# Kernel optimization log

Measured on AMD Instinct MI355X. Metric: run time of the kernel, lower is better.

## Reference

```python
import jax, jax.numpy as jnp
import numpy as np

BETA = 0.25
NUM_EMBEDDINGS = 512
DIM_EMBEDDING = 64


def setup_inputs() -> dict:
    key = jax.random.key(0)
    k1, k2 = jax.random.split(key)
    z_e = jax.random.normal(k1, (32, 64, 64, 64), dtype=jnp.float32)
    # torch init: uniform_(-1/num_embeddings, 1/num_embeddings)
    lim = 1.0 / NUM_EMBEDDINGS
    embeddings = jax.random.uniform(
        k2, (NUM_EMBEDDINGS, DIM_EMBEDDING), dtype=jnp.float32,
        minval=-lim, maxval=lim)
    return {"z_e": z_e, "embeddings": embeddings}


def reference(z_e, embeddings):
    # Flatten exactly as torch's z_e.view(-1, dim_embedding) on (N,C,H,W)
    z_flat = z_e.reshape(-1, DIM_EMBEDDING)          # [M, D]
    # Squared euclidean distances: ||z||^2 + ||e||^2 - 2 z e^T
    distances = (
        jnp.sum(z_flat ** 2, axis=1, keepdims=True)
        + jnp.sum(embeddings ** 2, axis=1)
        - 2.0 * jnp.matmul(z_flat, embeddings.T)
    )                                                # [M, K]
    encoding_indices = jnp.argmin(distances, axis=1)[:, None]  # [M, 1]
    quantized = embeddings[encoding_indices[:, 0]].reshape(z_e.shape)
    # Straight-through estimator
    quantized_st = z_e + jax.lax.stop_gradient(quantized - z_e)
    recon_loss = jnp.mean((jax.lax.stop_gradient(quantized_st) - z_e) ** 2)
    commitment_loss = BETA * jnp.mean(
        (quantized_st - jax.lax.stop_gradient(z_e)) ** 2)
    loss = recon_loss + commitment_loss
    return (loss, quantized_st, encoding_indices)
```

## Files before the change

### kernel.cpp

```cpp
#include <hip/hip_runtime.h>
#include <hip/hip_bf16.h>

constexpr int NELEM = 8388608;
constexpr int ROWS  = 64;
constexpr int NBLK  = 131072 / ROWS;
constexpr int ZS    = 68;
constexpr float EPS = 1e-3f;
constexpr int QCAP  = 1024;

typedef short bf16x8 __attribute__((ext_vector_type(8)));
typedef float v4f    __attribute__((ext_vector_type(4)));

__device__ bf16x8 g_efrag[32][2][64];
__device__ float  g_en2[512];

__device__ inline bf16x8 cvt_hi8(const float* __restrict__ s, float scale) {
    bf16x8 h;
#pragma unroll
    for (int j = 0; j < 8; ++j) {
        __hip_bfloat16 b = __float2bfloat16(scale * s[j]);
        h[j] = (short)__bfloat16_as_ushort(b);
    }
    return h;
}

__global__ void __launch_bounds__(256) vq_prep(const float* __restrict__ emb,
                                               float* __restrict__ out) {
    const int b = blockIdx.x;
    if (b < 16) {
        const int id   = b * 256 + threadIdx.x;
        const int lane = id & 63;
        const int kc   = (id >> 6) & 1;
        const int ct   = id >> 7;
        const float* src = emb + (size_t)(ct * 16 + (lane & 15)) * 64
                               + kc * 32 + (lane >> 4) * 8;
        g_efrag[ct][kc][lane] = cvt_hi8(src, -2.0f);
    } else {
#pragma unroll
        for (int c = 0; c < 2; ++c) {
            const int k = threadIdx.x + c * 256;
            const float4* e4 = (const float4*)(emb + (size_t)k * 64);
            float a = 0.f, bq = 0.f, cc = 0.f, d = 0.f;
#pragma unroll
            for (int i = 0; i < 16; ++i) {
                float4 v = e4[i];
                a += v.x * v.x; bq += v.y * v.y; cc += v.z * v.z; d += v.w * v.w;
            }
            g_en2[k] = (a + bq) + (cc + d);
        }
        if (threadIdx.x == 0) out[0] = 0.f;
    }
}

__global__ __launch_bounds__(256) __attribute__((amdgpu_waves_per_eu(4, 4)))
void vq_main(const float* __restrict__ z,
             const float* __restrict__ emb,
             float* __restrict__ out) {
    __shared__ float s_z[ROWS * ZS];
    __shared__ float s_en2[512];
    __shared__ float s_zn2[ROWS];
    __shared__ unsigned long long s_key[ROWS];
    __shared__ float s_wmin[ROWS][4];
    __shared__ float s_thr[ROWS];
    __shared__ unsigned s_q[QCAP];
    __shared__ int s_qn;
    __shared__ float s_lpart[4];

    const int tid  = threadIdx.x;
    const int lane = tid & 63;
    const int wid  = __builtin_amdgcn_readfirstlane(tid >> 6);
    const int mcol = lane & 15;
    const int quad = lane >> 4;

    {
        const int row = tid >> 2, seg = tid & 3;
        const float4* gp = (const float4*)(z + ((size_t)blockIdx.x * ROWS + row) * 64 + seg * 16);
#pragma unroll
        for (int i = 0; i < 4; ++i)
            *(float4*)&s_z[row * ZS + seg * 16 + i * 4] = gp[i];
    }
    s_en2[tid]       = g_en2[tid];
    s_en2[tid + 256] = g_en2[tid + 256];
    if (tid < ROWS) s_key[tid] = ~0ULL;
    if (tid == 0) s_qn = 0;
    __syncthreads();

    {
        const int row = tid >> 2, s = tid & 3;
        const float* zr = &s_z[row * ZS];
        float p = 0.f;
#pragma unroll
        for (int i = 0; i < 16; ++i) p += zr[4 * i + s] * zr[4 * i + s];
        p += __shfl_xor(p, 1, 64);
        p += __shfl_xor(p, 2, 64);
        if (s == 0) s_zn2[row] = p;
    }

    bf16x8 zf[4][2];
#pragma unroll
    for (int rg = 0; rg < 4; ++rg) {
        zf[rg][0] = cvt_hi8(&s_z[(rg * 16 + mcol) * ZS +  0 + quad * 8], 1.0f);
        zf[rg][1] = cvt_hi8(&s_z[(rg * 16 + mcol) * ZS + 32 + quad * 8], 1.0f);
    }

    float lmin[4];
#pragma unroll
    for (int rg = 0; rg < 4; ++rg) lmin[rg] = 3.402823466e38f;
#pragma unroll 2
    for (int ct = 0; ct < 8; ++ct) {
        const int gct = wid * 8 + ct;
        bf16x8 e0 = g_efrag[gct][0][lane];
        bf16x8 e1 = g_efrag[gct][1][lane];
        v4f base = *(const v4f*)&s_en2[gct * 16 + quad * 4];
#pragma unroll
        for (int rg = 0; rg < 4; ++rg) {
            v4f a = base;
            a = __builtin_amdgcn_mfma_f32_16x16x32_bf16(e0, zf[rg][0], a, 0, 0, 0);
            a = __builtin_amdgcn_mfma_f32_16x16x32_bf16(e1, zf[rg][1], a, 0, 0, 0);
            lmin[rg] = fminf(lmin[rg], fminf(fminf(a.x, a.y), fminf(a.z, a.w)));
        }
    }

#pragma unroll
    for (int rg = 0; rg < 4; ++rg) {
        float m = lmin[rg];
        m = fminf(m, __shfl_xor(m, 16, 64));
        m = fminf(m, __shfl_xor(m, 32, 64));
        if (quad == 0) s_wmin[rg * 16 + mcol][wid] = m;
    }
    __syncthreads();
    if (tid < ROWS)
        s_thr[tid] = fminf(fminf(s_wmin[tid][0], s_wmin[tid][1]),
                           fminf(s_wmin[tid][2], s_wmin[tid][3])) + EPS;
    __syncthreads();

    float thr[4];
#pragma unroll
    for (int rg = 0; rg < 4; ++rg) thr[rg] = s_thr[rg * 16 + mcol];
#pragma unroll 2
    for (int ct = 0; ct < 8; ++ct) {
        const int gct = wid * 8 + ct;
        bf16x8 e0 = g_efrag[gct][0][lane];
        bf16x8 e1 = g_efrag[gct][1][lane];
        v4f base = *(const v4f*)&s_en2[gct * 16 + quad * 4];
#pragma unroll
        for (int rg = 0; rg < 4; ++rg) {
            v4f a = base;
            a = __builtin_amdgcn_mfma_f32_16x16x32_bf16(e0, zf[rg][0], a, 0, 0, 0);
            a = __builtin_amdgcn_mfma_f32_16x16x32_bf16(e1, zf[rg][1], a, 0, 0, 0);
            float m4 = fminf(fminf(a.x, a.y), fminf(a.z, a.w));
            if (m4 <= thr[rg]) {
#pragma unroll
                for (int r = 0; r < 4; ++r) {
                    if (a[r] <= thr[rg]) {
                        int slot = atomicAdd(&s_qn, 1);
                        if (slot < QCAP)
                            s_q[slot] = ((unsigned)(rg * 16 + mcol) << 16) |
                                        (unsigned)(wid * 128 + ct * 16 + quad * 4 + r);
                    }
                }
            }
        }
    }
    __syncthreads();

    {
        const int qn = s_qn;
        for (int i = tid; i < qn && i < QCAP; i += 256) {
            const unsigned e = s_q[i];
            const int row = e >> 16, code = e & 0xFFFF;
            const float* zr = &s_z[row * ZS];
            const float* er = emb + (size_t)code * 64;
            float a = 0.f, b = 0.f, c2 = 0.f, d = 0.f;
#pragma unroll
            for (int g = 0; g < 16; ++g) {
                a  += zr[4*g]   * er[4*g];   b += zr[4*g+1] * er[4*g+1];
                c2 += zr[4*g+2] * er[4*g+2]; d += zr[4*g+3] * er[4*g+3];
            }
            float dot  = (a + b) + (c2 + d);
            float dist = (s_zn2[row] + s_en2[code]) - 2.0f * dot;
            unsigned long long key =
                ((unsigned long long)__float_as_uint(dist) << 32) | (unsigned)code;
            atomicMin(&s_key[row], key);
        }
    }
    __syncthreads();

    const int row = tid >> 2, seg = tid & 3;
    const int widx = (int)(unsigned)(s_key[row] & 0x1FFULL);
    const float* er = emb + (size_t)widx * 64 + seg * 16;
    const float* zr = &s_z[row * ZS + seg * 16];
    float* qo = out + 1 + ((size_t)blockIdx.x * ROWS + row) * 64 + seg * 16;
    float lsum = 0.f;
#pragma unroll
    for (int j = 0; j < 16; ++j) {
        float zv = zr[j], ev = er[j];
        float q = zv + (ev - zv);
        float df = q - zv; lsum += df * df;
        qo[j] = q;
    }
    if (seg == 0)
        out[1 + NELEM + blockIdx.x * ROWS + row] = (float)widx;

#pragma unroll
    for (int off = 32; off; off >>= 1) lsum += __shfl_down(lsum, off, 64);
    if (lane == 0) s_lpart[wid] = lsum;
    __syncthreads();
    if (tid == 0) {
        float p = (s_lpart[0] + s_lpart[1]) + (s_lpart[2] + s_lpart[3]);
        atomicAdd(out, p * (1.25f / 8388608.0f));
    }
}

extern "C" void kernel_launch(void* const* d_in, const int* in_sizes, int n_in,
                              void* d_out, int out_size, void* d_ws, size_t ws_size,
                              hipStream_t stream) {
    const float* z   = (const float*)d_in[0];
    const float* emb = (const float*)d_in[1];
    float* out = (float*)d_out;

    vq_prep<<<17, 256, 0, stream>>>(emb, out);
    vq_main<<<NBLK, 256, 0, stream>>>(z, emb, out);
}
```

Before: 131.3 us.

## Process four row tiles per block with register prefetch of next z tile

Each block now loops over four 64-row tiles instead of one, cutting the grid by 4x. The next tile's z data is loaded into registers at the start of each iteration and written to shared memory at the end, hiding global load latency behind the MFMA work. Occupancy hint drops from 4 to 2 waves per EU to allow more registers. The trade-off is fewer blocks to spread across CUs and lower occupancy for latency hiding.

```diff
diff --git a/kernel.cpp b/kernel.cpp
--- a/kernel.cpp
+++ b/kernel.cpp
@@ -3,7 +3,8 @@
 
 constexpr int NELEM = 8388608;
 constexpr int ROWS  = 64;
-constexpr int NBLK  = 131072 / ROWS;
+constexpr int TPB   = 4;
+constexpr int NBLK  = 131072 / ROWS / TPB;
 constexpr int ZS    = 68;
 constexpr float EPS = 1e-3f;
 constexpr int QCAP  = 1024;
@@ -52,7 +53,7 @@
     }
 }
 
-__global__ __launch_bounds__(256) __attribute__((amdgpu_waves_per_eu(4, 4)))
+__global__ __launch_bounds__(256) __attribute__((amdgpu_waves_per_eu(2, 2)))
 void vq_main(const float* __restrict__ z,
              const float* __restrict__ emb,
              float* __restrict__ out) {
@@ -71,144 +72,165 @@
     const int wid  = __builtin_amdgcn_readfirstlane(tid >> 6);
     const int mcol = lane & 15;
     const int quad = lane >> 4;
-
-    {
-        const int row = tid >> 2, seg = tid & 3;
-        const float4* gp = (const float4*)(z + ((size_t)blockIdx.x * ROWS + row) * 64 + seg * 16);
-#pragma unroll
-        for (int i = 0; i < 4; ++i)
-            *(float4*)&s_z[row * ZS + seg * 16 + i * 4] = gp[i];
-    }
+    const int row4 = tid >> 2, seg4 = tid & 3;
+
     s_en2[tid]       = g_en2[tid];
     s_en2[tid + 256] = g_en2[tid + 256];
+    {
+        const float4* gp = (const float4*)(z +
+            ((size_t)blockIdx.x * TPB * ROWS + row4) * 64 + seg4 * 16);
+#pragma unroll
+        for (int i = 0; i < 4; ++i)
+            *(float4*)&s_z[row4 * ZS + seg4 * 16 + i * 4] = gp[i];
+    }
     if (tid < ROWS) s_key[tid] = ~0ULL;
     if (tid == 0) s_qn = 0;
     __syncthreads();
 
-    {
-        const int row = tid >> 2, s = tid & 3;
-        const float* zr = &s_z[row * ZS];
-        float p = 0.f;
-#pragma unroll
-        for (int i = 0; i < 16; ++i) p += zr[4 * i + s] * zr[4 * i + s];
-        p += __shfl_xor(p, 1, 64);
-        p += __shfl_xor(p, 2, 64);
-        if (s == 0) s_zn2[row] = p;
-    }
-
-    bf16x8 zf[4][2];
-#pragma unroll
-    for (int rg = 0; rg < 4; ++rg) {
-        zf[rg][0] = cvt_hi8(&s_z[(rg * 16 + mcol) * ZS +  0 + quad * 8], 1.0f);
-        zf[rg][1] = cvt_hi8(&s_z[(rg * 16 + mcol) * ZS + 32 + quad * 8], 1.0f);
-    }
-
-    float lmin[4];
-#pragma unroll
-    for (int rg = 0; rg < 4; ++rg) lmin[rg] = 3.402823466e38f;
+    for (int t = 0; t < TPB; ++t) {
+        const size_t tbase = (size_t)(blockIdx.x * TPB + t) * ROWS;
+
+        float4 pf0, pf1, pf2, pf3;
+        if (t + 1 < TPB) {
+            const float4* gp = (const float4*)(z +
+                (tbase + ROWS + row4) * 64 + seg4 * 16);
+            pf0 = gp[0]; pf1 = gp[1]; pf2 = gp[2]; pf3 = gp[3];
+        }
+
+        {
+            const float* zr = &s_z[row4 * ZS];
+            float p = 0.f;
+#pragma unroll
+            for (int i = 0; i < 16; ++i) p += zr[4 * i + seg4] * zr[4 * i + seg4];
+            p += __shfl_xor(p, 1, 64);
+            p += __shfl_xor(p, 2, 64);
+            if (seg4 == 0) s_zn2[row4] = p;
+        }
+
+        bf16x8 zf[4][2];
+#pragma unroll
+        for (int rg = 0; rg < 4; ++rg) {
+            zf[rg][0] = cvt_hi8(&s_z[(rg * 16 + mcol) * ZS +  0 + quad * 8], 1.0f);
+            zf[rg][1] = cvt_hi8(&s_z[(rg * 16 + mcol) * ZS + 32 + quad * 8], 1.0f);
+        }
+
+        float lmin[4];
+#pragma unroll
+        for (int rg = 0; rg < 4; ++rg) lmin[rg] = 3.402823466e38f;
 #pragma unroll 2
-    for (int ct = 0; ct < 8; ++ct) {
-        const int gct = wid * 8 + ct;
-        bf16x8 e0 = g_efrag[gct][0][lane];
-        bf16x8 e1 = g_efrag[gct][1][lane];
-        v4f base = *(const v4f*)&s_en2[gct * 16 + quad * 4];
+        for (int ct = 0; ct < 8; ++ct) {
+            const int gct = wid * 8 + ct;
+            bf16x8 e0 = g_efrag[gct][0][lane];
+            bf16x8 e1 = g_efrag[gct][1][lane];
+            v4f base = *(const v4f*)&s_en2[gct * 16 + quad * 4];
+#pragma unroll
+            for (int rg = 0; rg < 4; ++rg) {
+                v4f a = base;
+                a = __builtin_amdgcn_mfma_f32_16x16x32_bf16(e0, zf[rg][0], a, 0, 0, 0);
+                a = __builtin_amdgcn_mfma_f32_16x16x32_bf16(e1, zf[rg][1], a, 0, 0, 0);
+                lmin[rg] = fminf(lmin[rg], fminf(fminf(a.x, a.y), fminf(a.z, a.w)));
+            }
+        }
+
 #pragma unroll
         for (int rg = 0; rg < 4; ++rg) {
-            v4f a = base;
-            a = __builtin_amdgcn_mfma_f32_16x16x32_bf16(e0, zf[rg][0], a, 0, 0, 0);
-            a = __builtin_amdgcn_mfma_f32_16x16x32_bf16(e1, zf[rg][1], a, 0, 0, 0);
-            lmin[rg] = fminf(lmin[rg], fminf(fminf(a.x, a.y), fminf(a.z, a.w)));
-        }
-    }
-
-#pragma unroll
-    for (int rg = 0; rg < 4; ++rg) {
-        float m = lmin[rg];
-        m = fminf(m, __shfl_xor(m, 16, 64));
-        m = fminf(m, __shfl_xor(m, 32, 64));
-        if (quad == 0) s_wmin[rg * 16 + mcol][wid] = m;
-    }
-    __syncthreads();
-    if (tid < ROWS)
-        s_thr[tid] = fminf(fminf(s_wmin[tid][0], s_wmin[tid][1]),
-                           fminf(s_wmin[tid][2], s_wmin[tid][3])) + EPS;
-    __syncthreads();
-
-    float thr[4];
-#pragma unroll
-    for (int rg = 0; rg < 4; ++rg) thr[rg] = s_thr[rg * 16 + mcol];
+            float m = lmin[rg];
+            m = fminf(m, __shfl_xor(m, 16, 64));
+            m = fminf(m, __shfl_xor(m, 32, 64));
+            if (quad == 0) s_wmin[rg * 16 + mcol][wid] = m;
+        }
+        __syncthreads();
+        if (tid < ROWS)
+            s_thr[tid] = fminf(fminf(s_wmin[tid][0], s_wmin[tid][1]),
+                               fminf(s_wmin[tid][2], s_wmin[tid][3])) + EPS;
+        __syncthreads();
+
+        float thr[4];
+#pragma unroll
+        for (int rg = 0; rg < 4; ++rg) thr[rg] = s_thr[rg * 16 + mcol];
 #pragma unroll 2
-    for (int ct = 0; ct < 8; ++ct) {
-        const int gct = wid * 8 + ct;
-        bf16x8 e0 = g_efrag[gct][0][lane];
-        bf16x8 e1 = g_efrag[gct][1][lane];
-        v4f base = *(const v4f*)&s_en2[gct * 16 + quad * 4];
-#pragma unroll
-        for (int rg = 0; rg < 4; ++rg) {
-            v4f a = base;
-            a = __builtin_amdgcn_mfma_f32_16x16x32_bf16(e0, zf[rg][0], a, 0, 0, 0);
-            a = __builtin_amdgcn_mfma_f32_16x16x32_bf16(e1, zf[rg][1], a, 0, 0, 0);
-            float m4 = fminf(fminf(a.x, a.y), fminf(a.z, a.w));
-            if (m4 <= thr[rg]) {
-#pragma unroll
-                for (int r = 0; r < 4; ++r) {
-                    if (a[r] <= thr[rg]) {
-                        int slot = atomicAdd(&s_qn, 1);
-                        if (slot < QCAP)
-                            s_q[slot] = ((unsigned)(rg * 16 + mcol) << 16) |
-                                        (unsigned)(wid * 128 + ct * 16 + quad * 4 + r);
+        for (int ct = 0; ct < 8; ++ct) {
+            const int gct = wid * 8 + ct;
+            bf16x8 e0 = g_efrag[gct][0][lane];
+            bf16x8 e1 = g_efrag[gct][1][lane];
+            v4f base = *(const v4f*)&s_en2[gct * 16 + quad * 4];
+#pragma unroll
+            for (int rg = 0; rg < 4; ++rg) {
+                v4f a = base;
+                a = __builtin_amdgcn_mfma_f32_16x16x32_bf16(e0, zf[rg][0], a, 0, 0, 0);
+                a = __builtin_amdgcn_mfma_f32_16x16x32_bf16(e1, zf[rg][1], a, 0, 0, 0);
+                float m4 = fminf(fminf(a.x, a.y), fminf(a.z, a.w));
+                if (m4 <= thr[rg]) {
+#pragma unroll
+                    for (int r = 0; r < 4; ++r) {
+                        if (a[r] <= thr[rg]) {
+                            int slot = atomicAdd(&s_qn, 1);
+                            if (slot < QCAP)
+                                s_q[slot] = ((unsigned)(rg * 16 + mcol) << 16) |
+                                            (unsigned)(wid * 128 + ct * 16 + quad * 4 + r);
+                        }
                     }
                 }
             }
         }
-    }
-    __syncthreads();
-
-    {
-        const int qn = s_qn;
-        for (int i = tid; i < qn && i < QCAP; i += 256) {
-            const unsigned e = s_q[i];
-            const int row = e >> 16, code = e & 0xFFFF;
-            const float* zr = &s_z[row * ZS];
-            const float* er = emb + (size_t)code * 64;
-            float a = 0.f, b = 0.f, c2 = 0.f, d = 0.f;
-#pragma unroll
-            for (int g = 0; g < 16; ++g) {
-                a  += zr[4*g]   * er[4*g];   b += zr[4*g+1] * er[4*g+1];
-                c2 += zr[4*g+2] * er[4*g+2]; d += zr[4*g+3] * er[4*g+3];
-            }
-            float dot  = (a + b) + (c2 + d);
-            float dist = (s_zn2[row] + s_en2[code]) - 2.0f * dot;
-            unsigned long long key =
-                ((unsigned long long)__float_as_uint(dist) << 32) | (unsigned)code;
-            atomicMin(&s_key[row], key);
-        }
-    }
-    __syncthreads();
-
-    const int row = tid >> 2, seg = tid & 3;
-    const int widx = (int)(unsigned)(s_key[row] & 0x1FFULL);
-    const float* er = emb + (size_t)widx * 64 + seg * 16;
-    const float* zr = &s_z[row * ZS + seg * 16];
-    float* qo = out + 1 + ((size_t)blockIdx.x * ROWS + row) * 64 + seg * 16;
-    float lsum = 0.f;
-#pragma unroll
-    for (int j = 0; j < 16; ++j) {
-        float zv = zr[j], ev = er[j];
-        float q = zv + (ev - zv);
-        float df = q - zv; lsum += df * df;
-        qo[j] = q;
-    }
-    if (seg == 0)
-        out[1 + NELEM + blockIdx.x * ROWS + row] = (float)widx;
-
-#pragma unroll
-    for (int off = 32; off; off >>= 1) lsum += __shfl_down(lsum, off, 64);
-    if (lane == 0) s_lpart[wid] = lsum;
-    __syncthreads();
-    if (tid == 0) {
-        float p = (s_lpart[0] + s_lpart[1]) + (s_lpart[2] + s_lpart[3]);
-        atomicAdd(out, p * (1.25f / 8388608.0f));
+        __syncthreads();
+
+        {
+            const int qn = s_qn;
+            for (int i = tid; i < qn && i < QCAP; i += 256) {
+                const unsigned e = s_q[i];
+                const int row = e >> 16, code = e & 0xFFFF;
+                const float* zr = &s_z[row * ZS];
+                const float* er = emb + (size_t)code * 64;
+                float a = 0.f, b = 0.f, c2 = 0.f, d = 0.f;
+#pragma unroll
+                for (int g = 0; g < 16; ++g) {
+                    a  += zr[4*g]   * er[4*g];   b += zr[4*g+1] * er[4*g+1];
+                    c2 += zr[4*g+2] * er[4*g+2]; d += zr[4*g+3] * er[4*g+3];
+                }
+                float dot  = (a + b) + (c2 + d);
+                float dist = (s_zn2[row] + s_en2[code]) - 2.0f * dot;
+                unsigned long long key =
+                    ((unsigned long long)__float_as_uint(dist) << 32) | (unsigned)code;
+                atomicMin(&s_key[row], key);
+            }
+        }
+        __syncthreads();
+
+        {
+            const int widx = (int)(unsigned)(s_key[row4] & 0x1FFULL);
+            const float* er = emb + (size_t)widx * 64 + seg4 * 16;
+            const float* zr = &s_z[row4 * ZS + seg4 * 16];
+            float* qo = out + 1 + (tbase + row4) * 64 + seg4 * 16;
+            float lsum = 0.f;
+#pragma unroll
+            for (int j = 0; j < 16; ++j) {
+                float zv = zr[j], ev = er[j];
+                float q = zv + (ev - zv);
+                float df = q - zv; lsum += df * df;
+                qo[j] = q;
+            }
+            if (seg4 == 0)
+                out[1 + NELEM + tbase + row4] = (float)widx;
+
+#pragma unroll
+            for (int off = 32; off; off >>= 1) lsum += __shfl_down(lsum, off, 64);
+            if (lane == 0) s_lpart[wid] = lsum;
+        }
+        __syncthreads();
+
+        if (tid == 0) {
+            float p = (s_lpart[0] + s_lpart[1]) + (s_lpart[2] + s_lpart[3]);
+            atomicAdd(out, p * (1.25f / 8388608.0f));
+            s_qn = 0;
+        }
+        if (tid < ROWS) s_key[tid] = ~0ULL;
+        if (t + 1 < TPB) {
+            float* d = &s_z[row4 * ZS + seg4 * 16];
+            *(float4*)&d[0]  = pf0;  *(float4*)&d[4]  = pf1;
+            *(float4*)&d[8]  = pf2;  *(float4*)&d[12] = pf3;
+        }
+        __syncthreads();
     }
 }
 
```

New measurement: 138.0 us. +5.1%, slower.
